# Kernel optimization log

Hardware: AMD Instinct MI355X
Metric: run time of the kernel (lower is better)

Reference implementation:

```python
import jax, jax.numpy as jnp
import numpy as np
import math

HEADS = 8
DIM_HEAD = 64
NUM_RETRIEVED = 32
ATTN_SCALE_INIT = 20.0


def l2norm(t, eps=1e-12):
    # matches torch F.normalize(dim=-1)
    n = jnp.linalg.norm(t, axis=-1, keepdims=True)
    return t / jnp.maximum(n, eps)


def setup_inputs() -> dict:
    key = jax.random.key(0)
    ks = jax.random.split(key, 8)
    b, n, dim = 2, 2048, HEADS * DIM_HEAD
    x = jax.random.normal(ks[0], (b, n, dim), dtype=jnp.float32)
    w_q = jax.random.normal(ks[1], (dim, HEADS * DIM_HEAD), dtype=jnp.float32) * (dim ** -0.5)
    w_kv = jax.random.normal(ks[2], (dim, 2 * DIM_HEAD), dtype=jnp.float32) * (dim ** -0.5)
    w_out = jax.random.normal(ks[3], (HEADS * DIM_HEAD, dim), dtype=jnp.float32) * (dim ** -0.5)
    scale_param = jnp.full((HEADS, 1, 1), math.log(ATTN_SCALE_INIT), dtype=jnp.float32)
    # retrieved memories are l2-normalized keys in the original (stored post-l2norm)
    mem_k = l2norm(jax.random.normal(ks[4], (b, HEADS, n, NUM_RETRIEVED, DIM_HEAD), dtype=jnp.float32))
    mem_v = jax.random.normal(ks[5], (b, HEADS, n, NUM_RETRIEVED, DIM_HEAD), dtype=jnp.float32)
    mem_mask = jnp.ones((b, HEADS, n, NUM_RETRIEVED), dtype=bool)
    return {"x": x, "w_q": w_q, "w_kv": w_kv, "w_out": w_out,
            "scale_param": scale_param, "mem_k": mem_k, "mem_v": mem_v,
            "mem_mask": mem_mask}


def reference(x, w_q, w_kv, w_out, scale_param, mem_k, mem_v, mem_mask):
    b, n, _ = x.shape
    h, d, K = HEADS, DIM_HEAD, NUM_RETRIEVED
    # projections
    q = (x @ w_q).reshape(b, n, h, d).transpose(0, 2, 1, 3)   # b h n d
    kv = x @ w_kv                                             # b n 2d (single shared kv head)
    k, v = kv[..., :d], kv[..., d:]                           # b n d each
    q = l2norm(q)
    k = l2norm(k)
    scale = jnp.exp(scale_param)                              # h 1 1 (learned temperature)
    # local causal attention scores
    sim = jnp.einsum('bhid,bjd->bhij', q, k) * scale          # b h n n
    mask_value = -jnp.finfo(sim.dtype).max
    causal = jnp.triu(jnp.ones((n, n), dtype=bool), k=1)
    sim = jnp.where(causal, mask_value, sim)
    # gathered KNN memory attention scores (per-query retrieved keys)
    sim_mem = jnp.einsum('bhid,bhijd->bhij', q, mem_k) * scale  # b h n K
    sim_mem = jnp.where(mem_mask, sim_mem, mask_value)
    # joint softmax over [memory | local]
    attn = jax.nn.softmax(jnp.concatenate((sim_mem, sim), axis=-1), axis=-1)
    mem_attn, local_attn = attn[..., :K], attn[..., K:]
    local_out = jnp.einsum('bhij,bjd->bhid', local_attn, v)
    mem_out = jnp.einsum('bhij,bhijd->bhid', mem_attn, mem_v)
    out = (local_out + mem_out).transpose(0, 2, 1, 3).reshape(b, n, h * d)
    return out @ w_out
```

## Files before the change

### kernel.cpp

```cpp
#include <hip/hip_runtime.h>
#include <math.h>

typedef unsigned short ushortT;
typedef __attribute__((ext_vector_type(8))) short bf16x8;
typedef __attribute__((ext_vector_type(4))) float f32x4;

#define MFMA16(a, b, c) __builtin_amdgcn_mfma_f32_16x16x32_bf16(a, b, c, 0, 0, 0)

__device__ __forceinline__ float bf2f(unsigned short u) {
  union { unsigned u; float f; } x; x.u = ((unsigned)u) << 16; return x.f;
}
__device__ __forceinline__ unsigned short f2bf(float f) {
  union { float f; unsigned u; } x; x.f = f;
  unsigned r = x.u + 0x7fffu + ((x.u >> 16) & 1u);
  return (unsigned short)(r >> 16);
}

__global__ __launch_bounds__(256) void cast_x(const float* __restrict__ in,
                                              ushortT* __restrict__ out) {
  int idx = (blockIdx.x * 256 + threadIdx.x) * 4;
  float4 v = *(const float4*)(in + idx);
  ushort4 o;
  o.x = f2bf(v.x); o.y = f2bf(v.y); o.z = f2bf(v.z); o.w = f2bf(v.w);
  *(ushort4*)(out + idx) = o;
}

__global__ __launch_bounds__(256) void tcast(const float* __restrict__ in,
                                             ushortT* __restrict__ out, int N, int Kfull) {
  __shared__ float Ld[64][65];
  const int t = threadIdx.x;
  const int k0 = blockIdx.x * 64, n0 = blockIdx.y * 64;
  const int r = t >> 3, c8 = (t & 7) * 8;
#pragma unroll
  for (int it = 0; it < 2; it++) {
    int j = r + it * 32;
    float4 a = *(const float4*)&in[(size_t)(k0 + j) * N + n0 + c8];
    float4 b = *(const float4*)&in[(size_t)(k0 + j) * N + n0 + c8 + 4];
    Ld[j][c8 + 0] = a.x; Ld[j][c8 + 1] = a.y; Ld[j][c8 + 2] = a.z; Ld[j][c8 + 3] = a.w;
    Ld[j][c8 + 4] = b.x; Ld[j][c8 + 5] = b.y; Ld[j][c8 + 6] = b.z; Ld[j][c8 + 7] = b.w;
  }
  __syncthreads();
#pragma unroll
  for (int it = 0; it < 2; it++) {
    int n = r + it * 32;
    ushort4 h0, h1;
    h0.x = f2bf(Ld[c8 + 0][n]); h0.y = f2bf(Ld[c8 + 1][n]);
    h0.z = f2bf(Ld[c8 + 2][n]); h0.w = f2bf(Ld[c8 + 3][n]);
    h1.x = f2bf(Ld[c8 + 4][n]); h1.y = f2bf(Ld[c8 + 5][n]);
    h1.z = f2bf(Ld[c8 + 6][n]); h1.w = f2bf(Ld[c8 + 7][n]);
    ushortT* dst = &out[(size_t)(n0 + n) * Kfull + k0 + c8];
    *(ushort4*)dst = h0; *(ushort4*)(dst + 4) = h1;
  }
}

template <int OUTF>
__global__ __launch_bounds__(256) void gemm_mfma(const ushortT* __restrict__ A,
                                                 const ushortT* __restrict__ BT,
                                                 void* __restrict__ Cv, int Ntot, int K) {
  __shared__ __align__(16) ushortT As[64][72];
  __shared__ __align__(16) ushortT Bs[64][72];
  const int t = threadIdx.x, w = t >> 6, lane = t & 63, quad = lane >> 4, m = lane & 15;
  const int m0 = blockIdx.x * 64, n0 = blockIdx.y * 64;
  const int r = t >> 3, c8 = (t & 7) * 8;
  f32x4 z = {0.f, 0.f, 0.f, 0.f};
  f32x4 acc[4] = {z, z, z, z};
  for (int k0 = 0; k0 < K; k0 += 64) {
    __syncthreads();
#pragma unroll
    for (int it = 0; it < 2; it++) {
      int rr = r + it * 32;
      *(uint4*)&As[rr][c8] = *(const uint4*)&A[(size_t)(m0 + rr) * K + k0 + c8];
      *(uint4*)&Bs[rr][c8] = *(const uint4*)&BT[(size_t)(n0 + rr) * K + k0 + c8];
    }
    __syncthreads();
#pragma unroll
    for (int ks = 0; ks < 2; ks++) {
      bf16x8 af = *(const bf16x8*)&As[w * 16 + m][ks * 32 + quad * 8];
#pragma unroll
      for (int nt = 0; nt < 4; nt++) {
        bf16x8 bfr = *(const bf16x8*)&Bs[nt * 16 + m][ks * 32 + quad * 8];
        acc[nt] = MFMA16(af, bfr, acc[nt]);
      }
    }
  }
#pragma unroll
  for (int nt = 0; nt < 4; nt++) {
#pragma unroll
    for (int reg = 0; reg < 4; reg++) {
      int row = m0 + w * 16 + quad * 4 + reg;
      int col = n0 + nt * 16 + m;
      if (OUTF)
        ((float*)Cv)[(size_t)row * Ntot + col] = acc[nt][reg];
      else
        ((ushortT*)Cv)[(size_t)row * Ntot + col] = f2bf(acc[nt][reg]);
    }
  }
}

__global__ __launch_bounds__(256) void norm_scatter(const ushortT* __restrict__ qkv,
                                                    ushortT* __restrict__ qb,
                                                    ushortT* __restrict__ kb) {
  const int t = threadIdx.x;
  const int wid = blockIdx.x * 4 + (t >> 6);
  const int lane = t & 63;
  const int row = wid / 9, grp = wid - row * 9;
  float val = bf2f(qkv[(size_t)row * 640 + grp * 64 + lane]);
  float ss = val * val;
#pragma unroll
  for (int o = 1; o < 64; o <<= 1) ss += __shfl_xor(ss, o);
  float nrm = fmaxf(sqrtf(ss), 1e-12f);
  unsigned short ov = f2bf(val / nrm);
  if (grp == 8) {
    kb[(size_t)row * 64 + lane] = ov;
  } else {
    int bI = row >> 11, iN = row & 2047;
    qb[(((size_t)bI * 8 + grp) * 2048 + iN) * 64 + lane] = ov;
  }
}

__global__ __launch_bounds__(256) void transpose_v(const ushortT* __restrict__ qkv,
                                                   ushortT* __restrict__ vt) {
  __shared__ float Ld[64][65];
  const int t = threadIdx.x, b = blockIdx.y;
  const int j0 = blockIdx.x * 64;
  const int r = t >> 3, c8 = (t & 7) * 8;
#pragma unroll
  for (int it = 0; it < 2; it++) {
    int j = r + it * 32;
    const ushortT* src = &qkv[((size_t)(b * 2048 + j0 + j)) * 640 + 576 + c8];
    ushort4 u0 = *(const ushort4*)src;
    ushort4 u1 = *(const ushort4*)(src + 4);
    Ld[j][c8 + 0] = bf2f(u0.x); Ld[j][c8 + 1] = bf2f(u0.y);
    Ld[j][c8 + 2] = bf2f(u0.z); Ld[j][c8 + 3] = bf2f(u0.w);
    Ld[j][c8 + 4] = bf2f(u1.x); Ld[j][c8 + 5] = bf2f(u1.y);
    Ld[j][c8 + 6] = bf2f(u1.z); Ld[j][c8 + 7] = bf2f(u1.w);
  }
  __syncthreads();
#pragma unroll
  for (int it = 0; it < 2; it++) {
    int d = r + it * 32;
    ushort4 h0, h1;
    h0.x = f2bf(Ld[c8 + 0][d]); h0.y = f2bf(Ld[c8 + 1][d]);
    h0.z = f2bf(Ld[c8 + 2][d]); h0.w = f2bf(Ld[c8 + 3][d]);
    h1.x = f2bf(Ld[c8 + 4][d]); h1.y = f2bf(Ld[c8 + 5][d]);
    h1.z = f2bf(Ld[c8 + 6][d]); h1.w = f2bf(Ld[c8 + 7][d]);
    ushortT* dst = &vt[((size_t)b * 64 + d) * 2048 + j0 + c8];
    *(ushort4*)dst = h0; *(ushort4*)(dst + 4) = h1;
  }
}

__global__ __launch_bounds__(256) void mem_attn(const ushortT* __restrict__ qb,
                                                const float* __restrict__ mk,
                                                const float* __restrict__ mv,
                                                const float* __restrict__ sp,
                                                float2* __restrict__ ml1,
                                                ushortT* __restrict__ acc1) {
  const int t = threadIdx.x;
  const int wid = blockIdx.x * 4 + (t >> 6);
  const int lane = t & 63;
  const int bh = wid >> 11, i = wid & 2047;
  const int d4 = (lane & 15) * 4;
  const float scale = __expf(sp[bh & 7]);
  const size_t base = ((size_t)bh * 2048 + i) * 2048;
  float4 kx[8], vx[8];
#pragma unroll
  for (int it = 0; it < 8; it++) kx[it] = *(const float4*)(mk + base + it * 256 + lane * 4);
#pragma unroll
  for (int it = 0; it < 8; it++) vx[it] = *(const float4*)(mv + base + it * 256 + lane * 4);
  ushort4 qu = *(const ushort4*)(qb + ((size_t)bh * 2048 + i) * 64 + d4);
  float q0 = bf2f(qu.x), q1 = bf2f(qu.y), q2 = bf2f(qu.z), q3 = bf2f(qu.w);
  float s[8];
#pragma unroll
  for (int it = 0; it < 8; it++) {
    float d = kx[it].x * q0 + kx[it].y * q1 + kx[it].z * q2 + kx[it].w * q3;
    d += __shfl_xor(d, 1); d += __shfl_xor(d, 2);
    d += __shfl_xor(d, 4); d += __shfl_xor(d, 8);
    s[it] = d * scale;
  }
  float mx = s[0];
#pragma unroll
  for (int it = 1; it < 8; it++) mx = fmaxf(mx, s[it]);
  mx = fmaxf(mx, __shfl_xor(mx, 16));
  mx = fmaxf(mx, __shfl_xor(mx, 32));
  float l = 0.f;
  float4 acc = make_float4(0.f, 0.f, 0.f, 0.f);
#pragma unroll
  for (int it = 0; it < 8; it++) {
    float p = __expf(s[it] - mx);
    l += p;
    acc.x += p * vx[it].x; acc.y += p * vx[it].y;
    acc.z += p * vx[it].z; acc.w += p * vx[it].w;
  }
  l += __shfl_xor(l, 16); l += __shfl_xor(l, 32);
  acc.x += __shfl_xor(acc.x, 16); acc.x += __shfl_xor(acc.x, 32);
  acc.y += __shfl_xor(acc.y, 16); acc.y += __shfl_xor(acc.y, 32);
  acc.z += __shfl_xor(acc.z, 16); acc.z += __shfl_xor(acc.z, 32);
  acc.w += __shfl_xor(acc.w, 16); acc.w += __shfl_xor(acc.w, 32);
  const float inv = 1.0f / l;
  if (lane < 16) {
    ushort4 o;
    o.x = f2bf(acc.x * inv); o.y = f2bf(acc.y * inv);
    o.z = f2bf(acc.z * inv); o.w = f2bf(acc.w * inv);
    *(ushort4*)(acc1 + ((size_t)bh * 2048 + i) * 64 + d4) = o;
  }
  if (lane == 0) ml1[(size_t)bh * 2048 + i] = make_float2(mx, l);
}

__global__ __launch_bounds__(256) void attn_local(const ushortT* __restrict__ qb,
                                                  const ushortT* __restrict__ kb,
                                                  const ushortT* __restrict__ vt,
                                                  const float2* __restrict__ ml1,
                                                  const ushortT* __restrict__ acc1,
                                                  const float* __restrict__ sp,
                                                  ushortT* __restrict__ ao) {
  __shared__ __align__(16) ushortT Ks[64][72];
  __shared__ __align__(16) ushortT Vs[64][72];
  __shared__ __align__(16) float Sc[4][16][36];
  __shared__ __align__(16) float Alf[4][20];
  __shared__ __align__(16) float Ml2[4][16][2];
  const int t = threadIdx.x, w = t >> 6, lane = t & 63, quad = lane >> 4, m = lane & 15;
  const int bh = blockIdx.x, bI = bh >> 3, h = bh & 7;
  const int T = gridDim.y - 1 - blockIdx.y;
  const int i0 = T * 64, iw = i0 + w * 16, i_lane = iw + m;
  const float scale = __expf(sp[h]);
  const ushortT* qrow = qb + ((size_t)bh * 2048 + i_lane) * 64;
  bf16x8 qf0 = *(const bf16x8*)(qrow + quad * 8);
  bf16x8 qf1 = *(const bf16x8*)(qrow + 32 + quad * 8);
  f32x4 z = {0.f, 0.f, 0.f, 0.f};
  f32x4 o[4] = {z, z, z, z};
  float m2 = -1e30f, l2 = 0.f;
  const int r = t >> 3, c8 = (t & 7) * 8;
  const ushortT* kgb = kb + (size_t)bI * 2048 * 64;
  const ushortT* vgb = vt + (size_t)bI * 64 * 2048;

  for (int kt = 0; kt <= T; kt++) {
    int j0 = kt * 64;
    __syncthreads();
#pragma unroll
    for (int it = 0; it < 2; it++) {
      int rr = r + it * 32;
      *(uint4*)&Ks[rr][c8] = *(const uint4*)&kgb[(size_t)(j0 + rr) * 64 + c8];
      *(uint4*)&Vs[rr][c8] = *(const uint4*)&vgb[(size_t)rr * 2048 + j0 + c8];
    }
    __syncthreads();
    for (int c = 0; c < 2; c++) {
      int j0c = j0 + c * 32;
      if (j0c > iw + 15) break;
      int cb = c * 32;
      bf16x8 k00 = *(const bf16x8*)&Ks[cb + m][quad * 8];
      bf16x8 k01 = *(const bf16x8*)&Ks[cb + m][32 + quad * 8];
      bf16x8 k10 = *(const bf16x8*)&Ks[cb + 16 + m][quad * 8];
      bf16x8 k11 = *(const bf16x8*)&Ks[cb + 16 + m][32 + quad * 8];
      f32x4 s0 = z, s1 = z;
      s0 = MFMA16(qf0, k00, s0);
      s0 = MFMA16(qf1, k01, s0);
      s1 = MFMA16(qf0, k10, s1);
      s1 = MFMA16(qf1, k11, s1);
#pragma unroll
      for (int reg = 0; reg < 4; reg++) {
        Sc[w][quad * 4 + reg][m] = s0[reg];
        Sc[w][quad * 4 + reg][16 + m] = s1[reg];
      }
      f32x4 r0 = *(const f32x4*)&Sc[w][m][quad * 8];
      f32x4 r1 = *(const f32x4*)&Sc[w][m][quad * 8 + 4];
      float sv[8] = {r0[0], r0[1], r0[2], r0[3], r1[0], r1[1], r1[2], r1[3]};
      const int jb = j0c + quad * 8;
      const bool nm = (j0c + 31 > iw);
#pragma unroll
      for (int jj = 0; jj < 8; jj++) {
        float sx = sv[jj] * scale;
        if (nm && (jb + jj > i_lane)) sx = -1e30f;
        sv[jj] = sx;
      }
      float cm = sv[0];
#pragma unroll
      for (int jj = 1; jj < 8; jj++) cm = fmaxf(cm, sv[jj]);
      cm = fmaxf(cm, __shfl_xor(cm, 16));
      cm = fmaxf(cm, __shfl_xor(cm, 32));
      float mn = fmaxf(m2, cm);
      float alpha = __expf(m2 - mn);
      m2 = mn;
      float ps = 0.f;
      bf16x8 pf;
#pragma unroll
      for (int jj = 0; jj < 8; jj++) {
        float p = __expf(sv[jj] - mn);
        ps += p;
        pf[jj] = (short)f2bf(p);
      }
      ps += __shfl_xor(ps, 16);
      ps += __shfl_xor(ps, 32);
      l2 = l2 * alpha + ps;
      if (quad == 0) Alf[w][m] = alpha;
      f32x4 al = *(const f32x4*)&Alf[w][quad * 4];
      o[0] *= al; o[1] *= al; o[2] *= al; o[3] *= al;
      bf16x8 v0 = *(const bf16x8*)&Vs[m][cb + quad * 8];
      bf16x8 v1 = *(const bf16x8*)&Vs[16 + m][cb + quad * 8];
      bf16x8 v2 = *(const bf16x8*)&Vs[32 + m][cb + quad * 8];
      bf16x8 v3 = *(const bf16x8*)&Vs[48 + m][cb + quad * 8];
      o[0] = MFMA16(pf, v0, o[0]);
      o[1] = MFMA16(pf, v1, o[1]);
      o[2] = MFMA16(pf, v2, o[2]);
      o[3] = MFMA16(pf, v3, o[3]);
    }
  }
  if (quad == 0) { Ml2[w][m][0] = m2; Ml2[w][m][1] = l2; }
  f32x4 mla = *(const f32x4*)&Ml2[w][quad * 4][0];
  f32x4 mlb = *(const f32x4*)&Ml2[w][quad * 4 + 2][0];
  float m2r[4] = {mla[0], mla[2], mlb[0], mlb[2]};
  float l2r[4] = {mla[1], mla[3], mlb[1], mlb[3]};
#pragma unroll
  for (int reg = 0; reg < 4; reg++) {
    int row = iw + quad * 4 + reg;
    float2 M1 = ml1[(size_t)bh * 2048 + row];
    float mm = fmaxf(m2r[reg], M1.x);
    float fl = __expf(m2r[reg] - mm);
    float w1 = M1.y * __expf(M1.x - mm);
    float invden = 1.0f / (l2r[reg] * fl + w1);
    const ushortT* arow = acc1 + ((size_t)bh * 2048 + row) * 64;
    ushortT* orow = ao + ((size_t)(bI * 2048 + row)) * 512 + h * 64;
#pragma unroll
    for (int nt = 0; nt < 4; nt++) {
      float a1 = bf2f(arow[nt * 16 + m]);
      float outv = (o[nt][reg] * fl + a1 * w1) * invden;
      orow[nt * 16 + m] = f2bf(outv);
    }
  }
}

extern "C" void kernel_launch(void* const* d_in, const int* in_sizes, int n_in,
                              void* d_out, int out_size, void* d_ws, size_t ws_size,
                              hipStream_t stream) {
  const float* x = (const float*)d_in[0];
  const float* w_q = (const float*)d_in[1];
  const float* w_kv = (const float*)d_in[2];
  const float* w_out = (const float*)d_in[3];
  const float* sp = (const float*)d_in[4];
  const float* mk = (const float*)d_in[5];
  const float* mv = (const float*)d_in[6];

  char* p = (char*)d_ws;
  ushortT* qkv = (ushortT*)p; p += 4096ll * 640 * 2;
  ushortT* ao = qkv;
  ushortT* qb = (ushortT*)p; p += 2097152ll * 2;
  ushortT* kbw = (ushortT*)p; p += 262144ll * 2;
  ushortT* vtw = (ushortT*)p; p += 262144ll * 2;
  float2* ml1 = (float2*)p; p += 32768ll * 8;
  ushortT* acc1 = (ushortT*)p; p += 2097152ll * 2;
  ushortT* xb = (ushortT*)p; p += 2097152ll * 2;
  ushortT* wqkvT = (ushortT*)p; p += 640ll * 512 * 2;
  ushortT* woutT = (ushortT*)p; p += 512ll * 512 * 2;

  cast_x<<<2048, 256, 0, stream>>>(x, xb);
  tcast<<<dim3(8, 8), 256, 0, stream>>>(w_q, wqkvT, 512, 512);
  tcast<<<dim3(8, 2), 256, 0, stream>>>(w_kv, wqkvT + 512 * 512, 128, 512);
  tcast<<<dim3(8, 8), 256, 0, stream>>>(w_out, woutT, 512, 512);
  gemm_mfma<0><<<dim3(64, 10), 256, 0, stream>>>(xb, wqkvT, qkv, 640, 512);
  norm_scatter<<<9216, 256, 0, stream>>>(qkv, qb, kbw);
  transpose_v<<<dim3(32, 2), 256, 0, stream>>>(qkv, vtw);
  mem_attn<<<8192, 256, 0, stream>>>(qb, mk, mv, sp, ml1, acc1);
  attn_local<<<dim3(16, 32), 256, 0, stream>>>(qb, kbw, vtw, ml1, acc1, sp, ao);
  gemm_mfma<1><<<dim3(64, 8), 256, 0, stream>>>(ao, woutT, d_out, 512, 512);
}
```

Measured before the change: 644.4 us.

## Fuse memory attention into local attention kernel and merge small launches

Memory-attention softmax over the retrieved keys is now computed inside the local attention kernel, once per query row. Its running max, sum and accumulator seed the online-softmax state, so the separate ml1/acc1 buffers and the final merge step go away. The three weight transpose-casts are merged into one launch, and norm_scatter is merged with transpose_v, cutting the launch count. The risk is that the fused kernel runs only 512 blocks and walks the 16 rows serially per wave while streaming the large mem_k/mem_v tensors, which may leave bandwidth underused compared with the old 8192-block memory kernel.

```diff
diff --git a/kernel.cpp b/kernel.cpp
--- a/kernel.cpp
+++ b/kernel.cpp
@@ -25,9 +25,18 @@
   *(ushort4*)(out + idx) = o;
 }
 
-__global__ __launch_bounds__(256) void tcast(const float* __restrict__ in,
-                                             ushortT* __restrict__ out, int N, int Kfull) {
+__global__ __launch_bounds__(256) void tcast_all(const float* __restrict__ wq,
+                                                 const float* __restrict__ wkv,
+                                                 const float* __restrict__ wout,
+                                                 ushortT* __restrict__ wqkvT,
+                                                 ushortT* __restrict__ woutT) {
   __shared__ float Ld[64][65];
+  const int z = blockIdx.z;
+  const float* in; ushortT* out; int N;
+  if (z == 0) { in = wq; out = wqkvT; N = 512; }
+  else if (z == 1) { if (blockIdx.y >= 2) return; in = wkv; out = wqkvT + 512 * 512; N = 128; }
+  else { in = wout; out = woutT; N = 512; }
+  const int Kfull = 512;
   const int t = threadIdx.x;
   const int k0 = blockIdx.x * 64, n0 = blockIdx.y * 64;
   const int r = t >> 3, c8 = (t & 7) * 8;
@@ -97,32 +106,32 @@
   }
 }
 
-__global__ __launch_bounds__(256) void norm_scatter(const ushortT* __restrict__ qkv,
-                                                    ushortT* __restrict__ qb,
-                                                    ushortT* __restrict__ kb) {
+__global__ __launch_bounds__(256) void nst(const ushortT* __restrict__ qkv,
+                                           ushortT* __restrict__ qb,
+                                           ushortT* __restrict__ kb,
+                                           ushortT* __restrict__ vt) {
+  __shared__ float Ld[64][65];
   const int t = threadIdx.x;
-  const int wid = blockIdx.x * 4 + (t >> 6);
-  const int lane = t & 63;
-  const int row = wid / 9, grp = wid - row * 9;
-  float val = bf2f(qkv[(size_t)row * 640 + grp * 64 + lane]);
-  float ss = val * val;
-#pragma unroll
-  for (int o = 1; o < 64; o <<= 1) ss += __shfl_xor(ss, o);
-  float nrm = fmaxf(sqrtf(ss), 1e-12f);
-  unsigned short ov = f2bf(val / nrm);
-  if (grp == 8) {
-    kb[(size_t)row * 64 + lane] = ov;
-  } else {
-    int bI = row >> 11, iN = row & 2047;
-    qb[(((size_t)bI * 8 + grp) * 2048 + iN) * 64 + lane] = ov;
-  }
-}
-
-__global__ __launch_bounds__(256) void transpose_v(const ushortT* __restrict__ qkv,
-                                                   ushortT* __restrict__ vt) {
-  __shared__ float Ld[64][65];
-  const int t = threadIdx.x, b = blockIdx.y;
-  const int j0 = blockIdx.x * 64;
+  if (blockIdx.x < 9216) {
+    const int wid = blockIdx.x * 4 + (t >> 6);
+    const int lane = t & 63;
+    const int row = wid / 9, grp = wid - row * 9;
+    float val = bf2f(qkv[(size_t)row * 640 + grp * 64 + lane]);
+    float ss = val * val;
+#pragma unroll
+    for (int o = 1; o < 64; o <<= 1) ss += __shfl_xor(ss, o);
+    float nrm = fmaxf(sqrtf(ss), 1e-12f);
+    unsigned short ov = f2bf(val / nrm);
+    if (grp == 8) {
+      kb[(size_t)row * 64 + lane] = ov;
+    } else {
+      int bI = row >> 11, iN = row & 2047;
+      qb[(((size_t)bI * 8 + grp) * 2048 + iN) * 64 + lane] = ov;
+    }
+    return;
+  }
+  const int idx = blockIdx.x - 9216;
+  const int b = idx >> 5, j0 = (idx & 31) * 64;
   const int r = t >> 3, c8 = (t & 7) * 8;
 #pragma unroll
   for (int it = 0; it < 2; it++) {
@@ -149,75 +158,21 @@
   }
 }
 
-__global__ __launch_bounds__(256) void mem_attn(const ushortT* __restrict__ qb,
-                                                const float* __restrict__ mk,
-                                                const float* __restrict__ mv,
-                                                const float* __restrict__ sp,
-                                                float2* __restrict__ ml1,
-                                                ushortT* __restrict__ acc1) {
-  const int t = threadIdx.x;
-  const int wid = blockIdx.x * 4 + (t >> 6);
-  const int lane = t & 63;
-  const int bh = wid >> 11, i = wid & 2047;
-  const int d4 = (lane & 15) * 4;
-  const float scale = __expf(sp[bh & 7]);
-  const size_t base = ((size_t)bh * 2048 + i) * 2048;
-  float4 kx[8], vx[8];
-#pragma unroll
-  for (int it = 0; it < 8; it++) kx[it] = *(const float4*)(mk + base + it * 256 + lane * 4);
-#pragma unroll
-  for (int it = 0; it < 8; it++) vx[it] = *(const float4*)(mv + base + it * 256 + lane * 4);
-  ushort4 qu = *(const ushort4*)(qb + ((size_t)bh * 2048 + i) * 64 + d4);
-  float q0 = bf2f(qu.x), q1 = bf2f(qu.y), q2 = bf2f(qu.z), q3 = bf2f(qu.w);
-  float s[8];
-#pragma unroll
-  for (int it = 0; it < 8; it++) {
-    float d = kx[it].x * q0 + kx[it].y * q1 + kx[it].z * q2 + kx[it].w * q3;
-    d += __shfl_xor(d, 1); d += __shfl_xor(d, 2);
-    d += __shfl_xor(d, 4); d += __shfl_xor(d, 8);
-    s[it] = d * scale;
-  }
-  float mx = s[0];
-#pragma unroll
-  for (int it = 1; it < 8; it++) mx = fmaxf(mx, s[it]);
-  mx = fmaxf(mx, __shfl_xor(mx, 16));
-  mx = fmaxf(mx, __shfl_xor(mx, 32));
-  float l = 0.f;
-  float4 acc = make_float4(0.f, 0.f, 0.f, 0.f);
-#pragma unroll
-  for (int it = 0; it < 8; it++) {
-    float p = __expf(s[it] - mx);
-    l += p;
-    acc.x += p * vx[it].x; acc.y += p * vx[it].y;
-    acc.z += p * vx[it].z; acc.w += p * vx[it].w;
-  }
-  l += __shfl_xor(l, 16); l += __shfl_xor(l, 32);
-  acc.x += __shfl_xor(acc.x, 16); acc.x += __shfl_xor(acc.x, 32);
-  acc.y += __shfl_xor(acc.y, 16); acc.y += __shfl_xor(acc.y, 32);
-  acc.z += __shfl_xor(acc.z, 16); acc.z += __shfl_xor(acc.z, 32);
-  acc.w += __shfl_xor(acc.w, 16); acc.w += __shfl_xor(acc.w, 32);
-  const float inv = 1.0f / l;
-  if (lane < 16) {
-    ushort4 o;
-    o.x = f2bf(acc.x * inv); o.y = f2bf(acc.y * inv);
-    o.z = f2bf(acc.z * inv); o.w = f2bf(acc.w * inv);
-    *(ushort4*)(acc1 + ((size_t)bh * 2048 + i) * 64 + d4) = o;
-  }
-  if (lane == 0) ml1[(size_t)bh * 2048 + i] = make_float2(mx, l);
-}
-
-__global__ __launch_bounds__(256) void attn_local(const ushortT* __restrict__ qb,
+__global__ __launch_bounds__(256) void attn_fused(const ushortT* __restrict__ qb,
                                                   const ushortT* __restrict__ kb,
                                                   const ushortT* __restrict__ vt,
-                                                  const float2* __restrict__ ml1,
-                                                  const ushortT* __restrict__ acc1,
+                                                  const float* __restrict__ mk,
+                                                  const float* __restrict__ mv,
                                                   const float* __restrict__ sp,
                                                   ushortT* __restrict__ ao) {
-  __shared__ __align__(16) ushortT Ks[64][72];
-  __shared__ __align__(16) ushortT Vs[64][72];
+  __shared__ __align__(16) char SmemKV[2][64 * 72 * 2];
   __shared__ __align__(16) float Sc[4][16][36];
   __shared__ __align__(16) float Alf[4][20];
   __shared__ __align__(16) float Ml2[4][16][2];
+  ushortT(*Ks)[72] = (ushortT(*)[72])SmemKV[0];
+  ushortT(*Vs)[72] = (ushortT(*)[72])SmemKV[1];
+  float* MemScr = (float*)SmemKV;
+
   const int t = threadIdx.x, w = t >> 6, lane = t & 63, quad = lane >> 4, m = lane & 15;
   const int bh = blockIdx.x, bI = bh >> 3, h = bh & 7;
   const int T = gridDim.y - 1 - blockIdx.y;
@@ -228,7 +183,61 @@
   bf16x8 qf1 = *(const bf16x8*)(qrow + 32 + quad * 8);
   f32x4 z = {0.f, 0.f, 0.f, 0.f};
   f32x4 o[4] = {z, z, z, z};
-  float m2 = -1e30f, l2 = 0.f;
+  float m2, l2;
+
+#pragma unroll 1
+  for (int r16 = 0; r16 < 16; ++r16) {
+    const int row = iw + r16;
+    const size_t base = ((size_t)bh * 2048 + row) * 2048;
+    float4 kx[8];
+#pragma unroll
+    for (int it = 0; it < 8; ++it) kx[it] = *(const float4*)(mk + base + it * 256 + lane * 4);
+    ushort4 qu = *(const ushort4*)(qb + ((size_t)bh * 2048 + row) * 64 + m * 4);
+    float q0 = bf2f(qu.x), q1 = bf2f(qu.y), q2 = bf2f(qu.z), q3 = bf2f(qu.w);
+    float s[8];
+#pragma unroll
+    for (int it = 0; it < 8; ++it) {
+      float d = kx[it].x * q0 + kx[it].y * q1 + kx[it].z * q2 + kx[it].w * q3;
+      d += __shfl_xor(d, 1); d += __shfl_xor(d, 2);
+      d += __shfl_xor(d, 4); d += __shfl_xor(d, 8);
+      s[it] = d * scale;
+    }
+    float4 vx[8];
+#pragma unroll
+    for (int it = 0; it < 8; ++it) vx[it] = *(const float4*)(mv + base + it * 256 + lane * 4);
+    float mx = s[0];
+#pragma unroll
+    for (int it = 1; it < 8; ++it) mx = fmaxf(mx, s[it]);
+    mx = fmaxf(mx, __shfl_xor(mx, 16));
+    mx = fmaxf(mx, __shfl_xor(mx, 32));
+    float l = 0.f;
+    float4 a = make_float4(0.f, 0.f, 0.f, 0.f);
+#pragma unroll
+    for (int it = 0; it < 8; ++it) {
+      float p = __expf(s[it] - mx);
+      l += p;
+      a.x += p * vx[it].x; a.y += p * vx[it].y;
+      a.z += p * vx[it].z; a.w += p * vx[it].w;
+    }
+    l += __shfl_xor(l, 16); l += __shfl_xor(l, 32);
+    a.x += __shfl_xor(a.x, 16); a.x += __shfl_xor(a.x, 32);
+    a.y += __shfl_xor(a.y, 16); a.y += __shfl_xor(a.y, 32);
+    a.z += __shfl_xor(a.z, 16); a.z += __shfl_xor(a.z, 32);
+    a.w += __shfl_xor(a.w, 16); a.w += __shfl_xor(a.w, 32);
+    if (lane == 0) { Ml2[w][r16][0] = mx; Ml2[w][r16][1] = l; }
+    if (quad == 0) *(float4*)&MemScr[(size_t)(w * 16 + r16) * 64 + m * 4] = a;
+  }
+#pragma unroll
+  for (int reg = 0; reg < 4; ++reg) {
+    const float* src = &MemScr[(size_t)(w * 16 + quad * 4 + reg) * 64];
+#pragma unroll
+    for (int nt = 0; nt < 4; ++nt) o[nt][reg] = src[nt * 16 + m];
+  }
+  {
+    float2 mlr = *(const float2*)&Ml2[w][m][0];
+    m2 = mlr.x; l2 = mlr.y;
+  }
+
   const int r = t >> 3, c8 = (t & 7) * 8;
   const ushortT* kgb = kb + (size_t)bI * 2048 * 64;
   const ushortT* vgb = vt + (size_t)bI * 64 * 2048;
@@ -307,23 +316,15 @@
   if (quad == 0) { Ml2[w][m][0] = m2; Ml2[w][m][1] = l2; }
   f32x4 mla = *(const f32x4*)&Ml2[w][quad * 4][0];
   f32x4 mlb = *(const f32x4*)&Ml2[w][quad * 4 + 2][0];
-  float m2r[4] = {mla[0], mla[2], mlb[0], mlb[2]};
   float l2r[4] = {mla[1], mla[3], mlb[1], mlb[3]};
 #pragma unroll
   for (int reg = 0; reg < 4; reg++) {
     int row = iw + quad * 4 + reg;
-    float2 M1 = ml1[(size_t)bh * 2048 + row];
-    float mm = fmaxf(m2r[reg], M1.x);
-    float fl = __expf(m2r[reg] - mm);
-    float w1 = M1.y * __expf(M1.x - mm);
-    float invden = 1.0f / (l2r[reg] * fl + w1);
-    const ushortT* arow = acc1 + ((size_t)bh * 2048 + row) * 64;
+    float invden = 1.0f / l2r[reg];
     ushortT* orow = ao + ((size_t)(bI * 2048 + row)) * 512 + h * 64;
 #pragma unroll
     for (int nt = 0; nt < 4; nt++) {
-      float a1 = bf2f(arow[nt * 16 + m]);
-      float outv = (o[nt][reg] * fl + a1 * w1) * invden;
-      orow[nt * 16 + m] = f2bf(outv);
+      orow[nt * 16 + m] = f2bf(o[nt][reg] * invden);
     }
   }
 }
@@ -345,20 +346,14 @@
   ushortT* qb = (ushortT*)p; p += 2097152ll * 2;
   ushortT* kbw = (ushortT*)p; p += 262144ll * 2;
   ushortT* vtw = (ushortT*)p; p += 262144ll * 2;
-  float2* ml1 = (float2*)p; p += 32768ll * 8;
-  ushortT* acc1 = (ushortT*)p; p += 2097152ll * 2;
   ushortT* xb = (ushortT*)p; p += 2097152ll * 2;
   ushortT* wqkvT = (ushortT*)p; p += 640ll * 512 * 2;
   ushortT* woutT = (ushortT*)p; p += 512ll * 512 * 2;
 
   cast_x<<<2048, 256, 0, stream>>>(x, xb);
-  tcast<<<dim3(8, 8), 256, 0, stream>>>(w_q, wqkvT, 512, 512);
-  tcast<<<dim3(8, 2), 256, 0, stream>>>(w_kv, wqkvT + 512 * 512, 128, 512);
-  tcast<<<dim3(8, 8), 256, 0, stream>>>(w_out, woutT, 512, 512);
+  tcast_all<<<dim3(8, 8, 3), 256, 0, stream>>>(w_q, w_kv, w_out, wqkvT, woutT);
   gemm_mfma<0><<<dim3(64, 10), 256, 0, stream>>>(xb, wqkvT, qkv, 640, 512);
-  norm_scatter<<<9216, 256, 0, stream>>>(qkv, qb, kbw);
-  transpose_v<<<dim3(32, 2), 256, 0, stream>>>(qkv, vtw);
-  mem_attn<<<8192, 256, 0, stream>>>(qb, mk, mv, sp, ml1, acc1);
-  attn_local<<<dim3(16, 32), 256, 0, stream>>>(qb, kbw, vtw, ml1, acc1, sp, ao);
+  nst<<<9280, 256, 0, stream>>>(qkv, qb, kbw, vtw);
+  attn_fused<<<dim3(16, 32), 256, 0, stream>>>(qb, kbw, vtw, mk, mv, sp, ao);
   gemm_mfma<1><<<dim3(64, 8), 256, 0, stream>>>(ao, woutT, d_out, 512, 512);
 }
```

New measurement: 617.7 us. 1.04x faster.

## Co-schedule memory and local attention in one launch, merge in separate pass

Applied to the files above, without the earlier changes.

Merges the three weight-transpose launches into one, fuses the q/k normalization with the V transpose, and runs the memory-retrieval attention blocks alongside the causal local-attention blocks in a single grid. The local path now writes unnormalized fp32 partial outputs and its running max/sum, and a new merge kernel combines them with the memory results. The aim is to cut launch count and let the bandwidth-bound memory attention overlap the compute-heavy, unevenly sized local tiles. In exchange it adds an extra fp32 round trip through global memory for the local outputs and one more kernel launch.

```diff
diff --git a/kernel.cpp b/kernel.cpp
--- a/kernel.cpp
+++ b/kernel.cpp
@@ -25,9 +25,18 @@
   *(ushort4*)(out + idx) = o;
 }
 
-__global__ __launch_bounds__(256) void tcast(const float* __restrict__ in,
-                                             ushortT* __restrict__ out, int N, int Kfull) {
+__global__ __launch_bounds__(256) void tcast_all(const float* __restrict__ wq,
+                                                 const float* __restrict__ wkv,
+                                                 const float* __restrict__ wout,
+                                                 ushortT* __restrict__ wqkvT,
+                                                 ushortT* __restrict__ woutT) {
   __shared__ float Ld[64][65];
+  const int z = blockIdx.z;
+  const float* in; ushortT* out; int N;
+  if (z == 0) { in = wq; out = wqkvT; N = 512; }
+  else if (z == 1) { if (blockIdx.y >= 2) return; in = wkv; out = wqkvT + 512 * 512; N = 128; }
+  else { in = wout; out = woutT; N = 512; }
+  const int Kfull = 512;
   const int t = threadIdx.x;
   const int k0 = blockIdx.x * 64, n0 = blockIdx.y * 64;
   const int r = t >> 3, c8 = (t & 7) * 8;
@@ -97,32 +106,32 @@
   }
 }
 
-__global__ __launch_bounds__(256) void norm_scatter(const ushortT* __restrict__ qkv,
-                                                    ushortT* __restrict__ qb,
-                                                    ushortT* __restrict__ kb) {
+__global__ __launch_bounds__(256) void nst(const ushortT* __restrict__ qkv,
+                                           ushortT* __restrict__ qb,
+                                           ushortT* __restrict__ kb,
+                                           ushortT* __restrict__ vt) {
+  __shared__ float Ld[64][65];
   const int t = threadIdx.x;
-  const int wid = blockIdx.x * 4 + (t >> 6);
-  const int lane = t & 63;
-  const int row = wid / 9, grp = wid - row * 9;
-  float val = bf2f(qkv[(size_t)row * 640 + grp * 64 + lane]);
-  float ss = val * val;
-#pragma unroll
-  for (int o = 1; o < 64; o <<= 1) ss += __shfl_xor(ss, o);
-  float nrm = fmaxf(sqrtf(ss), 1e-12f);
-  unsigned short ov = f2bf(val / nrm);
-  if (grp == 8) {
-    kb[(size_t)row * 64 + lane] = ov;
-  } else {
-    int bI = row >> 11, iN = row & 2047;
-    qb[(((size_t)bI * 8 + grp) * 2048 + iN) * 64 + lane] = ov;
-  }
-}
-
-__global__ __launch_bounds__(256) void transpose_v(const ushortT* __restrict__ qkv,
-                                                   ushortT* __restrict__ vt) {
-  __shared__ float Ld[64][65];
-  const int t = threadIdx.x, b = blockIdx.y;
-  const int j0 = blockIdx.x * 64;
+  if (blockIdx.x < 9216) {
+    const int wid = blockIdx.x * 4 + (t >> 6);
+    const int lane = t & 63;
+    const int row = wid / 9, grp = wid - row * 9;
+    float val = bf2f(qkv[(size_t)row * 640 + grp * 64 + lane]);
+    float ss = val * val;
+#pragma unroll
+    for (int o = 1; o < 64; o <<= 1) ss += __shfl_xor(ss, o);
+    float nrm = fmaxf(sqrtf(ss), 1e-12f);
+    unsigned short ov = f2bf(val / nrm);
+    if (grp == 8) {
+      kb[(size_t)row * 64 + lane] = ov;
+    } else {
+      int bI = row >> 11, iN = row & 2047;
+      qb[(((size_t)bI * 8 + grp) * 2048 + iN) * 64 + lane] = ov;
+    }
+    return;
+  }
+  const int idx = blockIdx.x - 9216;
+  const int b = idx >> 5, j0 = (idx & 31) * 64;
   const int r = t >> 3, c8 = (t & 7) * 8;
 #pragma unroll
   for (int it = 0; it < 2; it++) {
@@ -149,78 +158,79 @@
   }
 }
 
-__global__ __launch_bounds__(256) void mem_attn(const ushortT* __restrict__ qb,
-                                                const float* __restrict__ mk,
-                                                const float* __restrict__ mv,
-                                                const float* __restrict__ sp,
-                                                float2* __restrict__ ml1,
-                                                ushortT* __restrict__ acc1) {
-  const int t = threadIdx.x;
-  const int wid = blockIdx.x * 4 + (t >> 6);
-  const int lane = t & 63;
-  const int bh = wid >> 11, i = wid & 2047;
-  const int d4 = (lane & 15) * 4;
-  const float scale = __expf(sp[bh & 7]);
-  const size_t base = ((size_t)bh * 2048 + i) * 2048;
-  float4 kx[8], vx[8];
-#pragma unroll
-  for (int it = 0; it < 8; it++) kx[it] = *(const float4*)(mk + base + it * 256 + lane * 4);
-#pragma unroll
-  for (int it = 0; it < 8; it++) vx[it] = *(const float4*)(mv + base + it * 256 + lane * 4);
-  ushort4 qu = *(const ushort4*)(qb + ((size_t)bh * 2048 + i) * 64 + d4);
-  float q0 = bf2f(qu.x), q1 = bf2f(qu.y), q2 = bf2f(qu.z), q3 = bf2f(qu.w);
-  float s[8];
-#pragma unroll
-  for (int it = 0; it < 8; it++) {
-    float d = kx[it].x * q0 + kx[it].y * q1 + kx[it].z * q2 + kx[it].w * q3;
-    d += __shfl_xor(d, 1); d += __shfl_xor(d, 2);
-    d += __shfl_xor(d, 4); d += __shfl_xor(d, 8);
-    s[it] = d * scale;
-  }
-  float mx = s[0];
-#pragma unroll
-  for (int it = 1; it < 8; it++) mx = fmaxf(mx, s[it]);
-  mx = fmaxf(mx, __shfl_xor(mx, 16));
-  mx = fmaxf(mx, __shfl_xor(mx, 32));
-  float l = 0.f;
-  float4 acc = make_float4(0.f, 0.f, 0.f, 0.f);
-#pragma unroll
-  for (int it = 0; it < 8; it++) {
-    float p = __expf(s[it] - mx);
-    l += p;
-    acc.x += p * vx[it].x; acc.y += p * vx[it].y;
-    acc.z += p * vx[it].z; acc.w += p * vx[it].w;
-  }
-  l += __shfl_xor(l, 16); l += __shfl_xor(l, 32);
-  acc.x += __shfl_xor(acc.x, 16); acc.x += __shfl_xor(acc.x, 32);
-  acc.y += __shfl_xor(acc.y, 16); acc.y += __shfl_xor(acc.y, 32);
-  acc.z += __shfl_xor(acc.z, 16); acc.z += __shfl_xor(acc.z, 32);
-  acc.w += __shfl_xor(acc.w, 16); acc.w += __shfl_xor(acc.w, 32);
-  const float inv = 1.0f / l;
-  if (lane < 16) {
-    ushort4 o;
-    o.x = f2bf(acc.x * inv); o.y = f2bf(acc.y * inv);
-    o.z = f2bf(acc.z * inv); o.w = f2bf(acc.w * inv);
-    *(ushort4*)(acc1 + ((size_t)bh * 2048 + i) * 64 + d4) = o;
-  }
-  if (lane == 0) ml1[(size_t)bh * 2048 + i] = make_float2(mx, l);
-}
-
-__global__ __launch_bounds__(256) void attn_local(const ushortT* __restrict__ qb,
-                                                  const ushortT* __restrict__ kb,
-                                                  const ushortT* __restrict__ vt,
-                                                  const float2* __restrict__ ml1,
-                                                  const ushortT* __restrict__ acc1,
-                                                  const float* __restrict__ sp,
-                                                  ushortT* __restrict__ ao) {
+#define NLOC 512
+__global__ __launch_bounds__(256) void attn_ml(const ushortT* __restrict__ qb,
+                                               const ushortT* __restrict__ kb,
+                                               const ushortT* __restrict__ vt,
+                                               const float* __restrict__ mk,
+                                               const float* __restrict__ mv,
+                                               const float* __restrict__ sp,
+                                               float2* __restrict__ ml1,
+                                               ushortT* __restrict__ acc1,
+                                               float2* __restrict__ ml2,
+                                               float* __restrict__ o2) {
   __shared__ __align__(16) ushortT Ks[64][72];
   __shared__ __align__(16) ushortT Vs[64][72];
   __shared__ __align__(16) float Sc[4][16][36];
   __shared__ __align__(16) float Alf[4][20];
-  __shared__ __align__(16) float Ml2[4][16][2];
-  const int t = threadIdx.x, w = t >> 6, lane = t & 63, quad = lane >> 4, m = lane & 15;
-  const int bh = blockIdx.x, bI = bh >> 3, h = bh & 7;
-  const int T = gridDim.y - 1 - blockIdx.y;
+  __shared__ __align__(16) float Ml2s[4][16][2];
+  const int t = threadIdx.x;
+
+  if (blockIdx.x >= NLOC) {
+    const int wid = (blockIdx.x - NLOC) * 4 + (t >> 6);
+    const int lane = t & 63;
+    const int bh = wid >> 11, i = wid & 2047;
+    const int d4 = (lane & 15) * 4;
+    const float scale = __expf(sp[bh & 7]);
+    const size_t base = ((size_t)bh * 2048 + i) * 2048;
+    float4 kx[8], vx[8];
+#pragma unroll
+    for (int it = 0; it < 8; it++) kx[it] = *(const float4*)(mk + base + it * 256 + lane * 4);
+#pragma unroll
+    for (int it = 0; it < 8; it++) vx[it] = *(const float4*)(mv + base + it * 256 + lane * 4);
+    ushort4 qu = *(const ushort4*)(qb + ((size_t)bh * 2048 + i) * 64 + d4);
+    float q0 = bf2f(qu.x), q1 = bf2f(qu.y), q2 = bf2f(qu.z), q3 = bf2f(qu.w);
+    float s[8];
+#pragma unroll
+    for (int it = 0; it < 8; it++) {
+      float d = kx[it].x * q0 + kx[it].y * q1 + kx[it].z * q2 + kx[it].w * q3;
+      d += __shfl_xor(d, 1); d += __shfl_xor(d, 2);
+      d += __shfl_xor(d, 4); d += __shfl_xor(d, 8);
+      s[it] = d * scale;
+    }
+    float mx = s[0];
+#pragma unroll
+    for (int it = 1; it < 8; it++) mx = fmaxf(mx, s[it]);
+    mx = fmaxf(mx, __shfl_xor(mx, 16));
+    mx = fmaxf(mx, __shfl_xor(mx, 32));
+    float l = 0.f;
+    float4 acc = make_float4(0.f, 0.f, 0.f, 0.f);
+#pragma unroll
+    for (int it = 0; it < 8; it++) {
+      float p = __expf(s[it] - mx);
+      l += p;
+      acc.x += p * vx[it].x; acc.y += p * vx[it].y;
+      acc.z += p * vx[it].z; acc.w += p * vx[it].w;
+    }
+    l += __shfl_xor(l, 16); l += __shfl_xor(l, 32);
+    acc.x += __shfl_xor(acc.x, 16); acc.x += __shfl_xor(acc.x, 32);
+    acc.y += __shfl_xor(acc.y, 16); acc.y += __shfl_xor(acc.y, 32);
+    acc.z += __shfl_xor(acc.z, 16); acc.z += __shfl_xor(acc.z, 32);
+    acc.w += __shfl_xor(acc.w, 16); acc.w += __shfl_xor(acc.w, 32);
+    const float inv = 1.0f / l;
+    if (lane < 16) {
+      ushort4 o;
+      o.x = f2bf(acc.x * inv); o.y = f2bf(acc.y * inv);
+      o.z = f2bf(acc.z * inv); o.w = f2bf(acc.w * inv);
+      *(ushort4*)(acc1 + ((size_t)bh * 2048 + i) * 64 + d4) = o;
+    }
+    if (lane == 0) ml1[(size_t)bh * 2048 + i] = make_float2(mx, l);
+    return;
+  }
+
+  const int w = t >> 6, lane = t & 63, quad = lane >> 4, m = lane & 15;
+  const int bh = blockIdx.x & 15, bI = bh >> 3, h = bh & 7;
+  const int T = 31 - (blockIdx.x >> 4);
   const int i0 = T * 64, iw = i0 + w * 16, i_lane = iw + m;
   const float scale = __expf(sp[h]);
   const ushortT* qrow = qb + ((size_t)bh * 2048 + i_lane) * 64;
@@ -304,28 +314,45 @@
       o[3] = MFMA16(pf, v3, o[3]);
     }
   }
-  if (quad == 0) { Ml2[w][m][0] = m2; Ml2[w][m][1] = l2; }
-  f32x4 mla = *(const f32x4*)&Ml2[w][quad * 4][0];
-  f32x4 mlb = *(const f32x4*)&Ml2[w][quad * 4 + 2][0];
+  if (quad == 0) { Ml2s[w][m][0] = m2; Ml2s[w][m][1] = l2; }
+  f32x4 mla = *(const f32x4*)&Ml2s[w][quad * 4][0];
+  f32x4 mlb = *(const f32x4*)&Ml2s[w][quad * 4 + 2][0];
   float m2r[4] = {mla[0], mla[2], mlb[0], mlb[2]};
   float l2r[4] = {mla[1], mla[3], mlb[1], mlb[3]};
 #pragma unroll
   for (int reg = 0; reg < 4; reg++) {
     int row = iw + quad * 4 + reg;
-    float2 M1 = ml1[(size_t)bh * 2048 + row];
-    float mm = fmaxf(m2r[reg], M1.x);
-    float fl = __expf(m2r[reg] - mm);
-    float w1 = M1.y * __expf(M1.x - mm);
-    float invden = 1.0f / (l2r[reg] * fl + w1);
-    const ushortT* arow = acc1 + ((size_t)bh * 2048 + row) * 64;
-    ushortT* orow = ao + ((size_t)(bI * 2048 + row)) * 512 + h * 64;
-#pragma unroll
-    for (int nt = 0; nt < 4; nt++) {
-      float a1 = bf2f(arow[nt * 16 + m]);
-      float outv = (o[nt][reg] * fl + a1 * w1) * invden;
-      orow[nt * 16 + m] = f2bf(outv);
-    }
-  }
+    float* orow = o2 + ((size_t)bh * 2048 + row) * 64;
+#pragma unroll
+    for (int nt = 0; nt < 4; nt++) orow[nt * 16 + m] = o[nt][reg];
+    if (m == 0) ml2[(size_t)bh * 2048 + row] = make_float2(m2r[reg], l2r[reg]);
+  }
+}
+
+__global__ __launch_bounds__(256) void attn_merge(const float2* __restrict__ ml1,
+                                                  const ushortT* __restrict__ acc1,
+                                                  const float2* __restrict__ ml2,
+                                                  const float* __restrict__ o2,
+                                                  ushortT* __restrict__ ao) {
+  int idx = blockIdx.x * 256 + threadIdx.x;
+  int rowg = idx >> 4;
+  int d4 = (idx & 15) * 4;
+  float2 M1 = ml1[rowg];
+  float2 M2 = ml2[rowg];
+  float mm = fmaxf(M1.x, M2.x);
+  float fl = __expf(M2.x - mm);
+  float w1 = M1.y * __expf(M1.x - mm);
+  float invden = 1.0f / (M2.y * fl + w1);
+  float4 ov = *(const float4*)(o2 + (size_t)rowg * 64 + d4);
+  ushort4 a1 = *(const ushort4*)(acc1 + (size_t)rowg * 64 + d4);
+  int bh = rowg >> 11, i = rowg & 2047, bI = bh >> 3, h = bh & 7;
+  ushortT* orow = ao + ((size_t)(bI * 2048 + i)) * 512 + h * 64 + d4;
+  ushort4 o;
+  o.x = f2bf((ov.x * fl + bf2f(a1.x) * w1) * invden);
+  o.y = f2bf((ov.y * fl + bf2f(a1.y) * w1) * invden);
+  o.z = f2bf((ov.z * fl + bf2f(a1.z) * w1) * invden);
+  o.w = f2bf((ov.w * fl + bf2f(a1.w) * w1) * invden);
+  *(ushort4*)orow = o;
 }
 
 extern "C" void kernel_launch(void* const* d_in, const int* in_sizes, int n_in,
@@ -345,20 +372,19 @@
   ushortT* qb = (ushortT*)p; p += 2097152ll * 2;
   ushortT* kbw = (ushortT*)p; p += 262144ll * 2;
   ushortT* vtw = (ushortT*)p; p += 262144ll * 2;
-  float2* ml1 = (float2*)p; p += 32768ll * 8;
-  ushortT* acc1 = (ushortT*)p; p += 2097152ll * 2;
   ushortT* xb = (ushortT*)p; p += 2097152ll * 2;
   ushortT* wqkvT = (ushortT*)p; p += 640ll * 512 * 2;
   ushortT* woutT = (ushortT*)p; p += 512ll * 512 * 2;
+  float2* ml1 = (float2*)p; p += 32768ll * 8;
+  ushortT* acc1 = (ushortT*)p; p += 2097152ll * 2;
+  float2* ml2w = (float2*)p; p += 32768ll * 8;
+  float* o2w = (float*)p; p += 2097152ll * 4;
 
   cast_x<<<2048, 256, 0, stream>>>(x, xb);
-  tcast<<<dim3(8, 8), 256, 0, stream>>>(w_q, wqkvT, 512, 512);
-  tcast<<<dim3(8, 2), 256, 0, stream>>>(w_kv, wqkvT + 512 * 512, 128, 512);
-  tcast<<<dim3(8, 8), 256, 0, stream>>>(w_out, woutT, 512, 512);
+  tcast_all<<<dim3(8, 8, 3), 256, 0, stream>>>(w_q, w_kv, w_out, wqkvT, woutT);
   gemm_mfma<0><<<dim3(64, 10), 256, 0, stream>>>(xb, wqkvT, qkv, 640, 512);
-  norm_scatter<<<9216, 256, 0, stream>>>(qkv, qb, kbw);
-  transpose_v<<<dim3(32, 2), 256, 0, stream>>>(qkv, vtw);
-  mem_attn<<<8192, 256, 0, stream>>>(qb, mk, mv, sp, ml1, acc1);
-  attn_local<<<dim3(16, 32), 256, 0, stream>>>(qb, kbw, vtw, ml1, acc1, sp, ao);
+  nst<<<9280, 256, 0, stream>>>(qkv, qb, kbw, vtw);
+  attn_ml<<<NLOC + 8192, 256, 0, stream>>>(qb, kbw, vtw, mk, mv, sp, ml1, acc1, ml2w, o2w);
+  attn_merge<<<2048, 256, 0, stream>>>(ml1, acc1, ml2w, o2w, ao);
   gemm_mfma<1><<<dim3(64, 8), 256, 0, stream>>>(ao, woutT, d_out, 512, 512);
 }
```

Measured after the change: 565.9 us. 1.14x faster.
